# Kernel tuning notes

Measured on AMD Instinct MI355X. Metric: run time of the kernel, lower is better.

Reference implementation:

```python
import jax, jax.numpy as jnp
import numpy as np

B, T, H, W, D = 2, 8, 32, 32, 256
NUM_HEADS, KWIN_K = 8, 3
LN_EPS = 1e-5


def build_neighbor_idx(h, w, k):
    # Matches _build_indices: for each of N=h*w positions, the k*k clamped
    # (replicate-padded) neighbor flat indices. Returned as [N, k*k]
    # (already permuted like `idx.permute(1, 0)` in the torch forward).
    r = k // 2
    hh, ww = np.meshgrid(np.arange(h), np.arange(w), indexing='ij')
    nbrs = []
    for dh in range(-r, r + 1):
        for dw in range(-r, r + 1):
            nh = np.clip(hh + dh, 0, h - 1)
            nw = np.clip(ww + dw, 0, w - 1)
            nbrs.append((nh * w + nw).reshape(-1))
    return jnp.asarray(np.stack(nbrs, axis=1), dtype=jnp.int32)  # [N, k*k]


def setup_inputs() -> dict:
    key = jax.random.key(0)
    ks = jax.random.split(key, 9)
    s = 1.0 / np.sqrt(D)
    return {
        'x': jax.random.normal(ks[0], (B, T, H, W, D), dtype=jnp.float32),
        'ln_g': jnp.ones((D,), jnp.float32),
        'ln_b': jnp.zeros((D,), jnp.float32),
        'wq': jax.random.normal(ks[1], (D, D), jnp.float32) * s,
        'bq': jax.random.normal(ks[2], (D,), jnp.float32) * 0.01,
        'wk': jax.random.normal(ks[3], (D, D), jnp.float32) * s,
        'bk': jax.random.normal(ks[4], (D,), jnp.float32) * 0.01,
        'wv': jax.random.normal(ks[5], (D, D), jnp.float32) * s,
        'bv': jax.random.normal(ks[6], (D,), jnp.float32) * 0.01,
        'wo': jax.random.normal(ks[7], (D, D), jnp.float32) * s,
        'bo': jax.random.normal(ks[8], (D,), jnp.float32) * 0.01,
    }


def reference(x, ln_g, ln_b, wq, bq, wk, bk, wv, bv, wo, bo):
    # Dropout layers are identity (inference mode).
    b, t, h, w, d = x.shape
    n = h * w
    hd = d // NUM_HEADS
    x_ = x.reshape(b * t, n, d)

    # LayerNorm over last dim
    mu = jnp.mean(x_, axis=-1, keepdims=True)
    var = jnp.var(x_, axis=-1, keepdims=True)
    xn = (x_ - mu) * jax.lax.rsqrt(var + LN_EPS) * ln_g + ln_b

    q = xn @ wq + bq
    k_ = xn @ wk + bk
    v = xn @ wv + bv

    def split_heads(tns):  # [BT, N, D] -> [BT, heads, N, hd]
        return tns.reshape(b * t, n, NUM_HEADS, hd).transpose(0, 2, 1, 3)

    qh, kh, vh = split_heads(q), split_heads(k_), split_heads(v)

    idx = build_neighbor_idx(h, w, KWIN_K)  # [N, Kwin]
    # Gather neighbors directly (no expand): [BT, heads, N, Kwin, hd]
    k_local = kh[:, :, idx, :]
    v_local = vh[:, :, idx, :]

    scores = jnp.einsum('bhnd,bhnkd->bhnk', qh, k_local) / np.sqrt(hd)
    attn = jax.nn.softmax(scores, axis=-1)
    out = jnp.einsum('bhnk,bhnkd->bhnd', attn, v_local)

    out = out.transpose(0, 2, 1, 3).reshape(b * t, n, d)
    out = out @ wo + bo
    out = out + x_
    return out.reshape(b, t, h, w, d)
```

## Files before the change

### kernel.cpp

```cpp
#include <hip/hip_runtime.h>
#include <hip/hip_bf16.h>

#define M_TOT 16384
#define D_    256
#define K_DIM 256

typedef __attribute__((ext_vector_type(4))) float f32x4;
typedef __attribute__((ext_vector_type(8))) short s16x8;
typedef __attribute__((ext_vector_type(4))) short s16x4;

typedef const __attribute__((address_space(1))) void* gptr_t;
typedef __attribute__((address_space(3))) void* lptr_t;

__device__ __forceinline__ unsigned short f2bf(float f) {
  unsigned x = __float_as_uint(f);
  return (unsigned short)((x + 0x7fffu + ((x >> 16) & 1u)) >> 16);
}
__device__ __forceinline__ float bf2f(short s) {
  return __uint_as_float(((unsigned)(unsigned short)s) << 16);
}

__global__ __launch_bounds__(256) void prep_kernel(
    const float* __restrict__ x, const float* __restrict__ g, const float* __restrict__ b,
    unsigned short* __restrict__ xn,
    const float* __restrict__ wq, const float* __restrict__ wk,
    const float* __restrict__ wv, const float* __restrict__ wo,
    unsigned short* __restrict__ wt_qkv, unsigned short* __restrict__ wt_o) {
  __shared__ float tile[32][33];
  int tid = threadIdx.x;
  if (blockIdx.x < 4096) {
    int tok  = blockIdx.x * 4 + (tid >> 6);
    int lane = tid & 63;
    f32x4 v = ((const f32x4*)(x + (size_t)tok * D_))[lane];
    float s = 0.f, s2 = 0.f;
#pragma unroll
    for (int i = 0; i < 4; ++i) { s += v[i]; s2 += v[i] * v[i]; }
#pragma unroll
    for (int o = 1; o < 64; o <<= 1) { s += __shfl_xor(s, o); s2 += __shfl_xor(s2, o); }
    float mu   = s * (1.0f / 256.0f);
    float rstd = rsqrtf(s2 * (1.0f / 256.0f) - mu * mu + 1e-5f);
    f32x4 gv = ((const f32x4*)g)[lane];
    f32x4 bv = ((const f32x4*)b)[lane];
    s16x4 o4;
#pragma unroll
    for (int i = 0; i < 4; ++i) o4[i] = (short)f2bf((v[i] - mu) * rstd * gv[i] + bv[i]);
    ((s16x4*)(xn + (size_t)tok * D_))[lane] = o4;
  } else {
    int bid = blockIdx.x - 4096;
    int z   = bid >> 6;
    int rem = bid & 63;
    int k0 = (rem & 7) * 32, n0 = (rem >> 3) * 32;
    int tx = tid & 31, ty = tid >> 5;
    const float* src = (z == 0) ? wq : (z == 1) ? wk : (z == 2) ? wv : wo;
#pragma unroll
    for (int i = 0; i < 4; ++i) {
      int r = ty + i * 8;
      tile[r][tx] = src[(size_t)(k0 + r) * D_ + n0 + tx];
    }
    __syncthreads();
    unsigned short* dst = (z < 3) ? (wt_qkv + (size_t)(z * 256 + n0) * K_DIM + k0)
                                  : (wt_o + (size_t)n0 * K_DIM + k0);
#pragma unroll
    for (int i = 0; i < 4; ++i) {
      int r = ty + i * 8;
      dst[(size_t)r * K_DIM + tx] = f2bf(tile[tx][r]);
    }
  }
}

__global__ __launch_bounds__(256) void gemm_qkv_kernel(
    const unsigned short* __restrict__ A, const unsigned short* __restrict__ Bt,
    const float* __restrict__ b0, const float* __restrict__ b1, const float* __restrict__ b2,
    unsigned short* __restrict__ C) {
  __shared__ __align__(16) char smem[32768];
  char* Asm = smem;
  char* Bsm = smem + 16384;
  const int tid  = threadIdx.x;
  const int wid  = tid >> 6;
  const int lane = tid & 63;
  int lin = blockIdx.y * 6 + blockIdx.x;
  int swz = (lin & 7) * 96 + (lin >> 3);
  const int m0 = (swz / 6) * 128;
  const int n0 = (swz % 6) * 128;
  const int wave_m = wid >> 1;
  const int wave_n = wid & 1;

  f32x4 acc[4][4] = {};

  for (int ks = 0; ks < 4; ++ks) {
    const int kk0 = ks * 64;
    __syncthreads();
#pragma unroll
    for (int it = 0; it < 4; ++it) {
      int base     = (it * 256 + wid * 64) * 16;
      int lane_lin = base + lane * 16;
      int row  = lane_lin >> 7;
      int off  = lane_lin & 127;
      int soff = off ^ ((row & 7) << 4);
      const char* ga = (const char*)(A + (size_t)(m0 + row) * K_DIM + kk0) + soff;
      const char* gb = (const char*)(Bt + (size_t)(n0 + row) * K_DIM + kk0) + soff;
      __builtin_amdgcn_global_load_lds((gptr_t)ga, (lptr_t)(Asm + base), 16, 0, 0);
      __builtin_amdgcn_global_load_lds((gptr_t)gb, (lptr_t)(Bsm + base), 16, 0, 0);
    }
    __syncthreads();

#pragma unroll
    for (int kk = 0; kk < 2; ++kk) {
      s16x8 af[4], bf[4];
#pragma unroll
      for (int m = 0; m < 4; ++m) {
        int r    = wave_m * 64 + m * 16 + (lane & 15);
        int byte = kk * 64 + ((lane >> 4) * 16);
        af[m] = *(const s16x8*)(Asm + r * 128 + (byte ^ ((r & 7) << 4)));
      }
#pragma unroll
      for (int n = 0; n < 4; ++n) {
        int r    = wave_n * 64 + n * 16 + (lane & 15);
        int byte = kk * 64 + ((lane >> 4) * 16);
        bf[n] = *(const s16x8*)(Bsm + r * 128 + (byte ^ ((r & 7) << 4)));
      }
#pragma unroll
      for (int m = 0; m < 4; ++m)
#pragma unroll
        for (int n = 0; n < 4; ++n)
          acc[m][n] = __builtin_amdgcn_mfma_f32_16x16x32_bf16(af[m], bf[n], acc[m][n], 0, 0, 0);
    }
  }

  const int c0 = lane & 15;
  const int r0 = (lane >> 4) * 4;
#pragma unroll
  for (int m = 0; m < 4; ++m) {
#pragma unroll
    for (int n = 0; n < 4; ++n) {
      int row = m0 + wave_m * 64 + m * 16 + r0;
      int col = n0 + wave_n * 64 + n * 16 + c0;
      const float* bias = (col < 256) ? b0 : (col < 512) ? b1 : b2;
      float bb = bias[col & 255];
#pragma unroll
      for (int r = 0; r < 4; ++r)
        C[(size_t)(row + r) * 768 + col] = f2bf(acc[m][n][r] + bb);
    }
  }
}

__global__ __launch_bounds__(512) void attn_ogemm_kernel(
    const unsigned short* __restrict__ qkv, const unsigned short* __restrict__ wto,
    const float* __restrict__ bo, const float* __restrict__ x,
    float* __restrict__ out) {
  __shared__ __align__(16) char smem[65536];
  char* Asm = smem;
  char* Bsm = smem + 32768;
  const int tid  = threadIdx.x;
  const int wid  = tid >> 6;
  const int lane = tid & 63;
  const int m0 = blockIdx.x * 64;

#pragma unroll
  for (int t8 = 0; t8 < 8; ++t8) {
    int t   = wid * 8 + t8;
    int tok = m0 + t;
    int bt = tok >> 10;
    int n  = tok & 1023;
    int h  = n >> 5, w = n & 31;
    const size_t rowq = (size_t)tok * 768;
    s16x4 qr = *(const s16x4*)(qkv + rowq + lane * 4);
    f32x4 q;
#pragma unroll
    for (int i = 0; i < 4; ++i) q[i] = bf2f(qr[i]);

    f32x4 vst[9];
    float sc[9];
#pragma unroll
    for (int dh = -1; dh <= 1; ++dh) {
#pragma unroll
      for (int dw = -1; dw <= 1; ++dw) {
        const int j = (dh + 1) * 3 + (dw + 1);
        int nh = min(max(h + dh, 0), 31);
        int nw = min(max(w + dw, 0), 31);
        size_t nrow = (size_t)((bt << 10) + (nh << 5) + nw) * 768;
        s16x4 kr = *(const s16x4*)(qkv + nrow + 256 + lane * 4);
        s16x4 vr = *(const s16x4*)(qkv + nrow + 512 + lane * 4);
        float p = 0.f;
        f32x4 vv;
#pragma unroll
        for (int i = 0; i < 4; ++i) { p += q[i] * bf2f(kr[i]); vv[i] = bf2f(vr[i]); }
        p += __shfl_xor(p, 1);
        p += __shfl_xor(p, 2);
        p += __shfl_xor(p, 4);
        sc[j]  = p * 0.17677669529663687f;
        vst[j] = vv;
      }
    }
    float mx = sc[0];
#pragma unroll
    for (int j = 1; j < 9; ++j) mx = fmaxf(mx, sc[j]);
    float den = 0.f;
#pragma unroll
    for (int j = 0; j < 9; ++j) { sc[j] = __expf(sc[j] - mx); den += sc[j]; }
    float inv = 1.0f / den;
    f32x4 o = {};
#pragma unroll
    for (int j = 0; j < 9; ++j) {
      float wgt = sc[j] * inv;
#pragma unroll
      for (int i = 0; i < 4; ++i) o[i] += wgt * vst[j][i];
    }
    s16x4 ov;
#pragma unroll
    for (int i = 0; i < 4; ++i) ov[i] = (short)f2bf(o[i]);
    int byte = (lane * 8) ^ ((t & 7) << 4);
    *(s16x4*)(Asm + t * 512 + byte) = ov;
  }

  const int wave_m = wid >> 2;
  const int wave_n = wid & 3;
  f32x4 acc[2][4] = {};

  for (int ks = 0; ks < 4; ++ks) {
    __syncthreads();
#pragma unroll
    for (int it = 0; it < 4; ++it) {
      int base     = (it * 512 + wid * 64) * 16;
      int lane_lin = base + lane * 16;
      int row  = lane_lin >> 7;
      int off  = lane_lin & 127;
      int soff = off ^ ((row & 7) << 4);
      const char* gb = (const char*)(wto + (size_t)row * K_DIM + ks * 64) + soff;
      __builtin_amdgcn_global_load_lds((gptr_t)gb, (lptr_t)(Bsm + base), 16, 0, 0);
    }
    __syncthreads();

#pragma unroll
    for (int kk = 0; kk < 2; ++kk) {
      s16x8 af[2], bf[4];
#pragma unroll
      for (int m = 0; m < 2; ++m) {
        int r    = wave_m * 32 + m * 16 + (lane & 15);
        int byte = ks * 128 + kk * 64 + ((lane >> 4) * 16);
        af[m] = *(const s16x8*)(Asm + r * 512 + (byte ^ ((r & 7) << 4)));
      }
#pragma unroll
      for (int n = 0; n < 4; ++n) {
        int r    = wave_n * 64 + n * 16 + (lane & 15);
        int byte = kk * 64 + ((lane >> 4) * 16);
        bf[n] = *(const s16x8*)(Bsm + r * 128 + (byte ^ ((r & 7) << 4)));
      }
#pragma unroll
      for (int m = 0; m < 2; ++m)
#pragma unroll
        for (int n = 0; n < 4; ++n)
          acc[m][n] = __builtin_amdgcn_mfma_f32_16x16x32_bf16(af[m], bf[n], acc[m][n], 0, 0, 0);
    }
  }

  const int c0 = lane & 15;
  const int r0 = (lane >> 4) * 4;
#pragma unroll
  for (int m = 0; m < 2; ++m) {
#pragma unroll
    for (int n = 0; n < 4; ++n) {
      int row = m0 + wave_m * 32 + m * 16 + r0;
      int col = wave_n * 64 + n * 16 + c0;
      float bb = bo[col];
#pragma unroll
      for (int r = 0; r < 4; ++r)
        out[(size_t)(row + r) * D_ + col] =
            acc[m][n][r] + bb + x[(size_t)(row + r) * D_ + col];
    }
  }
}

extern "C" void kernel_launch(void* const* d_in, const int* in_sizes, int n_in,
                              void* d_out, int out_size, void* d_ws, size_t ws_size,
                              hipStream_t stream) {
  const float* x  = (const float*)d_in[0];
  const float* lg = (const float*)d_in[1];
  const float* lb = (const float*)d_in[2];
  const float* wq = (const float*)d_in[3];
  const float* bq = (const float*)d_in[4];
  const float* wk = (const float*)d_in[5];
  const float* bk = (const float*)d_in[6];
  const float* wv = (const float*)d_in[7];
  const float* bv = (const float*)d_in[8];
  const float* wo = (const float*)d_in[9];
  const float* bo = (const float*)d_in[10];
  float* out = (float*)d_out;

  char* ws = (char*)d_ws;
  unsigned short* xn    = (unsigned short*)ws;
  unsigned short* qkv   = (unsigned short*)(ws + 8388608);
  unsigned short* wtqkv = (unsigned short*)(ws + 33554432);
  unsigned short* wto   = (unsigned short*)(ws + 33947648);

  prep_kernel<<<4352, 256, 0, stream>>>(x, lg, lb, xn, wq, wk, wv, wo, wtqkv, wto);
  gemm_qkv_kernel<<<dim3(6, 128), 256, 0, stream>>>(xn, wtqkv, bq, bk, bv, qkv);
  attn_ogemm_kernel<<<256, 512, 0, stream>>>(qkv, wto, bo, x, out);
}
```

Baseline: 44.42 us.

## Stage K/V halo rows in LDS and assign one image row per block

The fused attention + output GEMM kernel now gives each block one image row of 32 tokens, with a swizzled block order, and launches 512 blocks instead of 256. It loads the 3-row K halo and then the V halo into shared memory with global_load_lds, and computes the softmax weights and weighted sums from LDS. Before, each token did 9 separate global neighbour reads. The change removes redundant global and L2 traffic for overlapping neighbours and doubles the number of blocks. In exchange it adds extra barriers, keeps weights for 4 tokens per wave in registers, and shrinks each wave's GEMM tile from 32x64 to 16x64.

```diff
diff --git a/kernel.cpp b/kernel.cpp
--- a/kernel.cpp
+++ b/kernel.cpp
@@ -149,47 +149,55 @@
     const float* __restrict__ bo, const float* __restrict__ x,
     float* __restrict__ out) {
   __shared__ __align__(16) char smem[65536];
-  char* Asm = smem;
-  char* Bsm = smem + 32768;
+  char* Halo = smem;
+  char* Asm  = smem + 49152;
   const int tid  = threadIdx.x;
   const int wid  = tid >> 6;
   const int lane = tid & 63;
-  const int m0 = blockIdx.x * 64;
-
-#pragma unroll
-  for (int t8 = 0; t8 < 8; ++t8) {
-    int t   = wid * 8 + t8;
-    int tok = m0 + t;
-    int bt = tok >> 10;
-    int n  = tok & 1023;
-    int h  = n >> 5, w = n & 31;
-    const size_t rowq = (size_t)tok * 768;
-    s16x4 qr = *(const s16x4*)(qkv + rowq + lane * 4);
+  int bswz = (blockIdx.x & 7) * 64 + (blockIdx.x >> 3);
+  const int bt = bswz >> 5;
+  const int h  = bswz & 31;
+  const int t0 = bswz * 32;
+  const size_t img = (size_t)bt << 10;
+
+  int srow[3];
+  srow[0] = max(h - 1, 0); srow[1] = h; srow[2] = min(h + 1, 31);
+
+#pragma unroll
+  for (int sweep = 0; sweep < 6; ++sweep) {
+    int chunk = sweep * 8 + wid;
+    int slot = chunk >> 4, t2 = chunk & 15;
+    int tokw = t2 * 2 + (lane >> 5);
+    int off  = (lane & 31) * 16;
+    size_t grow = img + (size_t)srow[slot] * 32 + tokw;
+    const char* ga = (const char*)qkv + grow * 1536 + 512 + off;
+    __builtin_amdgcn_global_load_lds((gptr_t)ga, (lptr_t)(Halo + chunk * 1024), 16, 0, 0);
+  }
+  __syncthreads();
+
+  float wgt[4][9];
+#pragma unroll
+  for (int i = 0; i < 4; ++i) {
+    int tloc = wid * 4 + i;
+    s16x4 qr = *(const s16x4*)(qkv + (size_t)(t0 + tloc) * 768 + lane * 4);
     f32x4 q;
 #pragma unroll
-    for (int i = 0; i < 4; ++i) q[i] = bf2f(qr[i]);
-
-    f32x4 vst[9];
+    for (int e = 0; e < 4; ++e) q[e] = bf2f(qr[e]);
     float sc[9];
 #pragma unroll
-    for (int dh = -1; dh <= 1; ++dh) {
+    for (int s = 0; s < 3; ++s) {
 #pragma unroll
       for (int dw = -1; dw <= 1; ++dw) {
-        const int j = (dh + 1) * 3 + (dw + 1);
-        int nh = min(max(h + dh, 0), 31);
-        int nw = min(max(w + dw, 0), 31);
-        size_t nrow = (size_t)((bt << 10) + (nh << 5) + nw) * 768;
-        s16x4 kr = *(const s16x4*)(qkv + nrow + 256 + lane * 4);
-        s16x4 vr = *(const s16x4*)(qkv + nrow + 512 + lane * 4);
+        const int j = s * 3 + (dw + 1);
+        int cw = min(max(tloc + dw, 0), 31);
+        s16x4 kr = *(const s16x4*)(Halo + (s * 32 + cw) * 512 + lane * 8);
         float p = 0.f;
-        f32x4 vv;
-#pragma unroll
-        for (int i = 0; i < 4; ++i) { p += q[i] * bf2f(kr[i]); vv[i] = bf2f(vr[i]); }
+#pragma unroll
+        for (int e = 0; e < 4; ++e) p += q[e] * bf2f(kr[e]);
         p += __shfl_xor(p, 1);
         p += __shfl_xor(p, 2);
         p += __shfl_xor(p, 4);
-        sc[j]  = p * 0.17677669529663687f;
-        vst[j] = vv;
+        sc[j] = p * 0.17677669529663687f;
       }
     }
     float mx = sc[0];
@@ -199,74 +207,94 @@
 #pragma unroll
     for (int j = 0; j < 9; ++j) { sc[j] = __expf(sc[j] - mx); den += sc[j]; }
     float inv = 1.0f / den;
+#pragma unroll
+    for (int j = 0; j < 9; ++j) wgt[i][j] = sc[j] * inv;
+  }
+  __syncthreads();
+
+#pragma unroll
+  for (int sweep = 0; sweep < 6; ++sweep) {
+    int chunk = sweep * 8 + wid;
+    int slot = chunk >> 4, t2 = chunk & 15;
+    int tokw = t2 * 2 + (lane >> 5);
+    int off  = (lane & 31) * 16;
+    size_t grow = img + (size_t)srow[slot] * 32 + tokw;
+    const char* ga = (const char*)qkv + grow * 1536 + 1024 + off;
+    __builtin_amdgcn_global_load_lds((gptr_t)ga, (lptr_t)(Halo + chunk * 1024), 16, 0, 0);
+  }
+  __syncthreads();
+
+#pragma unroll
+  for (int i = 0; i < 4; ++i) {
+    int tloc = wid * 4 + i;
     f32x4 o = {};
 #pragma unroll
-    for (int j = 0; j < 9; ++j) {
-      float wgt = sc[j] * inv;
-#pragma unroll
-      for (int i = 0; i < 4; ++i) o[i] += wgt * vst[j][i];
+    for (int s = 0; s < 3; ++s) {
+#pragma unroll
+      for (int dw = -1; dw <= 1; ++dw) {
+        const int j = s * 3 + (dw + 1);
+        int cw = min(max(tloc + dw, 0), 31);
+        s16x4 vr = *(const s16x4*)(Halo + (s * 32 + cw) * 512 + lane * 8);
+        float wj = wgt[i][j];
+#pragma unroll
+        for (int e = 0; e < 4; ++e) o[e] += wj * bf2f(vr[e]);
+      }
     }
     s16x4 ov;
 #pragma unroll
-    for (int i = 0; i < 4; ++i) ov[i] = (short)f2bf(o[i]);
-    int byte = (lane * 8) ^ ((t & 7) << 4);
-    *(s16x4*)(Asm + t * 512 + byte) = ov;
+    for (int e = 0; e < 4; ++e) ov[e] = (short)f2bf(o[e]);
+    int byte = (lane * 8) ^ ((tloc & 7) << 4);
+    *(s16x4*)(Asm + tloc * 512 + byte) = ov;
   }
 
   const int wave_m = wid >> 2;
   const int wave_n = wid & 3;
-  f32x4 acc[2][4] = {};
+  f32x4 acc[4] = {};
 
   for (int ks = 0; ks < 4; ++ks) {
     __syncthreads();
 #pragma unroll
     for (int it = 0; it < 4; ++it) {
-      int base     = (it * 512 + wid * 64) * 16;
+      int base     = it * 8192 + wid * 1024;
       int lane_lin = base + lane * 16;
       int row  = lane_lin >> 7;
       int off  = lane_lin & 127;
       int soff = off ^ ((row & 7) << 4);
       const char* gb = (const char*)(wto + (size_t)row * K_DIM + ks * 64) + soff;
-      __builtin_amdgcn_global_load_lds((gptr_t)gb, (lptr_t)(Bsm + base), 16, 0, 0);
+      __builtin_amdgcn_global_load_lds((gptr_t)gb, (lptr_t)(Halo + base), 16, 0, 0);
     }
     __syncthreads();
 
 #pragma unroll
     for (int kk = 0; kk < 2; ++kk) {
-      s16x8 af[2], bf[4];
-#pragma unroll
-      for (int m = 0; m < 2; ++m) {
-        int r    = wave_m * 32 + m * 16 + (lane & 15);
+      s16x8 af, bf[4];
+      {
+        int r    = wave_m * 16 + (lane & 15);
         int byte = ks * 128 + kk * 64 + ((lane >> 4) * 16);
-        af[m] = *(const s16x8*)(Asm + r * 512 + (byte ^ ((r & 7) << 4)));
+        af = *(const s16x8*)(Asm + r * 512 + (byte ^ ((r & 7) << 4)));
       }
 #pragma unroll
       for (int n = 0; n < 4; ++n) {
         int r    = wave_n * 64 + n * 16 + (lane & 15);
         int byte = kk * 64 + ((lane >> 4) * 16);
-        bf[n] = *(const s16x8*)(Bsm + r * 128 + (byte ^ ((r & 7) << 4)));
-      }
-#pragma unroll
-      for (int m = 0; m < 2; ++m)
-#pragma unroll
-        for (int n = 0; n < 4; ++n)
-          acc[m][n] = __builtin_amdgcn_mfma_f32_16x16x32_bf16(af[m], bf[n], acc[m][n], 0, 0, 0);
+        bf[n] = *(const s16x8*)(Halo + r * 128 + (byte ^ ((r & 7) << 4)));
+      }
+#pragma unroll
+      for (int n = 0; n < 4; ++n)
+        acc[n] = __builtin_amdgcn_mfma_f32_16x16x32_bf16(af, bf[n], acc[n], 0, 0, 0);
     }
   }
 
   const int c0 = lane & 15;
   const int r0 = (lane >> 4) * 4;
 #pragma unroll
-  for (int m = 0; m < 2; ++m) {
-#pragma unroll
-    for (int n = 0; n < 4; ++n) {
-      int row = m0 + wave_m * 32 + m * 16 + r0;
-      int col = wave_n * 64 + n * 16 + c0;
-      float bb = bo[col];
-#pragma unroll
-      for (int r = 0; r < 4; ++r)
-        out[(size_t)(row + r) * D_ + col] =
-            acc[m][n][r] + bb + x[(size_t)(row + r) * D_ + col];
+  for (int n = 0; n < 4; ++n) {
+    int col = wave_n * 64 + n * 16 + c0;
+    float bb = bo[col];
+#pragma unroll
+    for (int r = 0; r < 4; ++r) {
+      int row = t0 + wave_m * 16 + r0 + r;
+      out[(size_t)row * D_ + col] = acc[n][r] + bb + x[(size_t)row * D_ + col];
     }
   }
 }
@@ -295,5 +323,5 @@
 
   prep_kernel<<<4352, 256, 0, stream>>>(x, lg, lb, xn, wq, wk, wv, wo, wtqkv, wto);
   gemm_qkv_kernel<<<dim3(6, 128), 256, 0, stream>>>(xn, wtqkv, bq, bk, bv, qkv);
-  attn_ogemm_kernel<<<256, 512, 0, stream>>>(qkv, wto, bo, x, out);
-}
+  attn_ogemm_kernel<<<512, 512, 0, stream>>>(qkv, wto, bo, x, out);
+}
```

Measured after the change: 41.40 us. -6.8%, faster.

## Stage K/V halo rows in LDS for attention and double-buffer output-projection weights

Applied to the files above, without the earlier changes.

The attention kernel now assigns each block two image rows and first copies the K and V rows it needs (the two own rows plus one halo row above and below) into LDS with async global-to-LDS loads. Neighbour reads for the 3x3 window then come from LDS instead of repeated global gathers. The output-projection weight tiles are double-buffered so the next K slice loads while the MFMAs run. The QKV GEMM is retiled to 128x256 blocks with 512 threads. The attention kernel now needs 160KB of dynamic LDS, which allows only one block per CU.

```diff
diff --git a/kernel.cpp b/kernel.cpp
--- a/kernel.cpp
+++ b/kernel.cpp
@@ -68,22 +68,22 @@
   }
 }
 
-__global__ __launch_bounds__(256) void gemm_qkv_kernel(
+__global__ __launch_bounds__(512, 4) void gemm_qkv_kernel(
     const unsigned short* __restrict__ A, const unsigned short* __restrict__ Bt,
     const float* __restrict__ b0, const float* __restrict__ b1, const float* __restrict__ b2,
     unsigned short* __restrict__ C) {
-  __shared__ __align__(16) char smem[32768];
+  __shared__ __align__(16) char smem[49152];
   char* Asm = smem;
   char* Bsm = smem + 16384;
   const int tid  = threadIdx.x;
   const int wid  = tid >> 6;
   const int lane = tid & 63;
-  int lin = blockIdx.y * 6 + blockIdx.x;
-  int swz = (lin & 7) * 96 + (lin >> 3);
-  const int m0 = (swz / 6) * 128;
-  const int n0 = (swz % 6) * 128;
-  const int wave_m = wid >> 1;
-  const int wave_n = wid & 1;
+  int lin = blockIdx.x;
+  int swz = (lin & 7) * 48 + (lin >> 3);
+  const int m0 = (swz / 3) * 128;
+  const int n0 = (swz % 3) * 256;
+  const int wave_m = wid >> 2;
+  const int wave_n = wid & 3;
 
   f32x4 acc[4][4] = {};
 
@@ -91,15 +91,23 @@
     const int kk0 = ks * 64;
     __syncthreads();
 #pragma unroll
-    for (int it = 0; it < 4; ++it) {
-      int base     = (it * 256 + wid * 64) * 16;
+    for (int it = 0; it < 2; ++it) {
+      int base     = it * 8192 + wid * 1024;
       int lane_lin = base + lane * 16;
       int row  = lane_lin >> 7;
       int off  = lane_lin & 127;
       int soff = off ^ ((row & 7) << 4);
       const char* ga = (const char*)(A + (size_t)(m0 + row) * K_DIM + kk0) + soff;
+      __builtin_amdgcn_global_load_lds((gptr_t)ga, (lptr_t)(Asm + base), 16, 0, 0);
+    }
+#pragma unroll
+    for (int it = 0; it < 4; ++it) {
+      int base     = it * 8192 + wid * 1024;
+      int lane_lin = base + lane * 16;
+      int row  = lane_lin >> 7;
+      int off  = lane_lin & 127;
+      int soff = off ^ ((row & 7) << 4);
       const char* gb = (const char*)(Bt + (size_t)(n0 + row) * K_DIM + kk0) + soff;
-      __builtin_amdgcn_global_load_lds((gptr_t)ga, (lptr_t)(Asm + base), 16, 0, 0);
       __builtin_amdgcn_global_load_lds((gptr_t)gb, (lptr_t)(Bsm + base), 16, 0, 0);
     }
     __syncthreads();
@@ -148,48 +156,61 @@
     const unsigned short* __restrict__ qkv, const unsigned short* __restrict__ wto,
     const float* __restrict__ bo, const float* __restrict__ x,
     float* __restrict__ out) {
-  __shared__ __align__(16) char smem[65536];
-  char* Asm = smem;
-  char* Bsm = smem + 32768;
+  extern __shared__ __align__(16) char smem[];
+  char* KH   = smem;
+  char* VH   = smem + 65536;
+  char* Asm  = smem + 131072;
+  char* Bsm0 = smem;
+  char* Bsm1 = smem + 32768;
   const int tid  = threadIdx.x;
   const int wid  = tid >> 6;
   const int lane = tid & 63;
-  const int m0 = blockIdx.x * 64;
-
-#pragma unroll
-  for (int t8 = 0; t8 < 8; ++t8) {
-    int t   = wid * 8 + t8;
-    int tok = m0 + t;
-    int bt = tok >> 10;
-    int n  = tok & 1023;
-    int h  = n >> 5, w = n & 31;
-    const size_t rowq = (size_t)tok * 768;
-    s16x4 qr = *(const s16x4*)(qkv + rowq + lane * 4);
+  int bswz = (blockIdx.x & 7) * 32 + (blockIdx.x >> 3);
+  const int bt = bswz >> 4;
+  const int h0 = (bswz & 15) * 2;
+  const int t0 = bt * 1024 + h0 * 32;
+  const size_t img = (size_t)bt << 10;
+  int srow[4];
+  srow[0] = max(h0 - 1, 0); srow[1] = h0; srow[2] = h0 + 1; srow[3] = min(h0 + 2, 31);
+
+#pragma unroll
+  for (int i = 0; i < 8; ++i) {
+    int chunk = wid * 8 + i;
+    int tokw  = (chunk & 15) * 2 + (lane >> 5);
+    int off   = (lane & 31) * 16;
+    size_t grow = img + (size_t)srow[chunk >> 4] * 32 + tokw;
+    const char* gk = (const char*)qkv + grow * 1536 + 512 + off;
+    const char* gv = (const char*)qkv + grow * 1536 + 1024 + off;
+    __builtin_amdgcn_global_load_lds((gptr_t)gk, (lptr_t)(KH + chunk * 1024), 16, 0, 0);
+    __builtin_amdgcn_global_load_lds((gptr_t)gv, (lptr_t)(VH + chunk * 1024), 16, 0, 0);
+  }
+  __syncthreads();
+
+#pragma unroll
+  for (int i = 0; i < 8; ++i) {
+    int tloc = wid * 8 + i;
+    int hr = tloc >> 5;
+    int w  = tloc & 31;
+    s16x4 qr = *(const s16x4*)(qkv + (size_t)(t0 + tloc) * 768 + lane * 4);
     f32x4 q;
 #pragma unroll
-    for (int i = 0; i < 4; ++i) q[i] = bf2f(qr[i]);
-
-    f32x4 vst[9];
+    for (int e = 0; e < 4; ++e) q[e] = bf2f(qr[e]);
     float sc[9];
 #pragma unroll
-    for (int dh = -1; dh <= 1; ++dh) {
+    for (int ds = 0; ds < 3; ++ds) {
 #pragma unroll
       for (int dw = -1; dw <= 1; ++dw) {
-        const int j = (dh + 1) * 3 + (dw + 1);
-        int nh = min(max(h + dh, 0), 31);
-        int nw = min(max(w + dw, 0), 31);
-        size_t nrow = (size_t)((bt << 10) + (nh << 5) + nw) * 768;
-        s16x4 kr = *(const s16x4*)(qkv + nrow + 256 + lane * 4);
-        s16x4 vr = *(const s16x4*)(qkv + nrow + 512 + lane * 4);
+        const int j = ds * 3 + (dw + 1);
+        int cw   = min(max(w + dw, 0), 31);
+        int srel = hr + ds;
+        s16x4 kr = *(const s16x4*)(KH + (srel * 32 + cw) * 512 + lane * 8);
         float p = 0.f;
-        f32x4 vv;
-#pragma unroll
-        for (int i = 0; i < 4; ++i) { p += q[i] * bf2f(kr[i]); vv[i] = bf2f(vr[i]); }
+#pragma unroll
+        for (int e = 0; e < 4; ++e) p += q[e] * bf2f(kr[e]);
         p += __shfl_xor(p, 1);
         p += __shfl_xor(p, 2);
         p += __shfl_xor(p, 4);
-        sc[j]  = p * 0.17677669529663687f;
-        vst[j] = vv;
+        sc[j] = p * 0.17677669529663687f;
       }
     }
     float mx = sc[0];
@@ -201,36 +222,57 @@
     float inv = 1.0f / den;
     f32x4 o = {};
 #pragma unroll
-    for (int j = 0; j < 9; ++j) {
-      float wgt = sc[j] * inv;
-#pragma unroll
-      for (int i = 0; i < 4; ++i) o[i] += wgt * vst[j][i];
+    for (int ds = 0; ds < 3; ++ds) {
+#pragma unroll
+      for (int dw = -1; dw <= 1; ++dw) {
+        const int j = ds * 3 + (dw + 1);
+        int cw   = min(max(w + dw, 0), 31);
+        int srel = hr + ds;
+        s16x4 vr = *(const s16x4*)(VH + (srel * 32 + cw) * 512 + lane * 8);
+        float wj = sc[j] * inv;
+#pragma unroll
+        for (int e = 0; e < 4; ++e) o[e] += wj * bf2f(vr[e]);
+      }
     }
     s16x4 ov;
 #pragma unroll
-    for (int i = 0; i < 4; ++i) ov[i] = (short)f2bf(o[i]);
-    int byte = (lane * 8) ^ ((t & 7) << 4);
-    *(s16x4*)(Asm + t * 512 + byte) = ov;
-  }
+    for (int e = 0; e < 4; ++e) ov[e] = (short)f2bf(o[e]);
+    int byte = (lane * 8) ^ ((tloc & 7) << 4);
+    *(s16x4*)(Asm + tloc * 512 + byte) = ov;
+  }
+  __syncthreads();
 
   const int wave_m = wid >> 2;
   const int wave_n = wid & 3;
   f32x4 acc[2][4] = {};
 
+#pragma unroll
+  for (int it = 0; it < 4; ++it) {
+    int base     = it * 8192 + wid * 1024;
+    int lane_lin = base + lane * 16;
+    int row  = lane_lin >> 7;
+    int off  = lane_lin & 127;
+    int soff = off ^ ((row & 7) << 4);
+    const char* gb = (const char*)wto + (size_t)row * 512 + 0 * 128 + soff;
+    __builtin_amdgcn_global_load_lds((gptr_t)gb, (lptr_t)(Bsm0 + base), 16, 0, 0);
+  }
+  __syncthreads();
+
   for (int ks = 0; ks < 4; ++ks) {
-    __syncthreads();
-#pragma unroll
-    for (int it = 0; it < 4; ++it) {
-      int base     = (it * 512 + wid * 64) * 16;
-      int lane_lin = base + lane * 16;
-      int row  = lane_lin >> 7;
-      int off  = lane_lin & 127;
-      int soff = off ^ ((row & 7) << 4);
-      const char* gb = (const char*)(wto + (size_t)row * K_DIM + ks * 64) + soff;
-      __builtin_amdgcn_global_load_lds((gptr_t)gb, (lptr_t)(Bsm + base), 16, 0, 0);
-    }
-    __syncthreads();
-
+    if (ks < 3) {
+      char* dst = ((ks + 1) & 1) ? Bsm1 : Bsm0;
+#pragma unroll
+      for (int it = 0; it < 4; ++it) {
+        int base     = it * 8192 + wid * 1024;
+        int lane_lin = base + lane * 16;
+        int row  = lane_lin >> 7;
+        int off  = lane_lin & 127;
+        int soff = off ^ ((row & 7) << 4);
+        const char* gb = (const char*)wto + (size_t)row * 512 + (ks + 1) * 128 + soff;
+        __builtin_amdgcn_global_load_lds((gptr_t)gb, (lptr_t)(dst + base), 16, 0, 0);
+      }
+    }
+    char* buf = (ks & 1) ? Bsm1 : Bsm0;
 #pragma unroll
     for (int kk = 0; kk < 2; ++kk) {
       s16x8 af[2], bf[4];
@@ -244,7 +286,7 @@
       for (int n = 0; n < 4; ++n) {
         int r    = wave_n * 64 + n * 16 + (lane & 15);
         int byte = kk * 64 + ((lane >> 4) * 16);
-        bf[n] = *(const s16x8*)(Bsm + r * 128 + (byte ^ ((r & 7) << 4)));
+        bf[n] = *(const s16x8*)(buf + r * 128 + (byte ^ ((r & 7) << 4)));
       }
 #pragma unroll
       for (int m = 0; m < 2; ++m)
@@ -252,6 +294,7 @@
         for (int n = 0; n < 4; ++n)
           acc[m][n] = __builtin_amdgcn_mfma_f32_16x16x32_bf16(af[m], bf[n], acc[m][n], 0, 0, 0);
     }
+    __syncthreads();
   }
 
   const int c0 = lane & 15;
@@ -260,13 +303,13 @@
   for (int m = 0; m < 2; ++m) {
 #pragma unroll
     for (int n = 0; n < 4; ++n) {
-      int row = m0 + wave_m * 32 + m * 16 + r0;
       int col = wave_n * 64 + n * 16 + c0;
       float bb = bo[col];
 #pragma unroll
-      for (int r = 0; r < 4; ++r)
-        out[(size_t)(row + r) * D_ + col] =
-            acc[m][n][r] + bb + x[(size_t)(row + r) * D_ + col];
+      for (int r = 0; r < 4; ++r) {
+        int row = t0 + wave_m * 32 + m * 16 + r0 + r;
+        out[(size_t)row * D_ + col] = acc[m][n][r] + bb + x[(size_t)row * D_ + col];
+      }
     }
   }
 }
@@ -293,7 +336,10 @@
   unsigned short* wtqkv = (unsigned short*)(ws + 33554432);
   unsigned short* wto   = (unsigned short*)(ws + 33947648);
 
+  (void)hipFuncSetAttribute((const void*)attn_ogemm_kernel,
+                            hipFuncAttributeMaxDynamicSharedMemorySize, 163840);
+
   prep_kernel<<<4352, 256, 0, stream>>>(x, lg, lb, xn, wq, wk, wv, wo, wtqkv, wto);
-  gemm_qkv_kernel<<<dim3(6, 128), 256, 0, stream>>>(xn, wtqkv, bq, bk, bv, qkv);
-  attn_ogemm_kernel<<<256, 512, 0, stream>>>(qkv, wto, bo, x, out);
-}
+  gemm_qkv_kernel<<<384, 512, 0, stream>>>(xn, wtqkv, bq, bk, bv, qkv);
+  attn_ogemm_kernel<<<256, 512, 163840, stream>>>(qkv, wto, bo, x, out);
+}
```

New measurement: 55.47 us. 24.9% more time.
